# Kernel tuning notes

Hardware: AMD Instinct MI355X
Metric: run time of the kernel (lower is better)

## Reference

```python
import jax, jax.numpy as jnp
import numpy as np

NEG_INF = float('-inf')


def setup_inputs() -> dict:
    key = jax.random.key(0)
    ks = jax.random.split(key, 5)
    B, S, D = 2, 4096, 2048
    H, Hd, R = 16, 64, 64  # heads, head_dim, dq_rank
    ratio = 4
    sc = 0.02
    return {
        'hidden': jax.random.normal(ks[0], (B, S, D), jnp.float32),
        'w_dq': jax.random.normal(ks[1], (D, R), jnp.float32) * sc,
        'w_iuq': jax.random.normal(ks[2], (R, H * Hd), jnp.float32) * sc,
        'w_w': jax.random.normal(ks[3], (D, H), jnp.float32) * sc,
        'w_comp': jax.random.normal(ks[4], (ratio * D, Hd), jnp.float32) * sc,
        'compress_ratio': ratio,
        'index_topk': 256,
    }


def reference(hidden, w_dq, w_iuq, w_w, w_comp, compress_ratio, index_topk):
    B, S, D = hidden.shape
    r = int(compress_ratio)
    K = int(index_topk)
    P = S // r
    H = w_w.shape[1]
    Hd = w_iuq.shape[1] // H

    # mini-Compressor: linear over concatenated windows of r tokens -> [B,P,Hd]
    k_icomp = hidden.reshape(B, P, r * D) @ w_comp

    # low-rank query projection: [B,S,R] -> [B,S,H,Hd]
    q_i = ((hidden @ w_dq) @ w_iuq).reshape(B, S, H, Hd)
    w_i = hidden @ w_w  # [B,S,H]

    relu = jax.nn.relu(jnp.einsum('bshd,bpd->bshp', q_i, k_icomp))
    scores = jnp.einsum('bshp,bsh->bsp', relu, w_i)  # weighted head-sum

    # causal mask over compressed pool: pool s covers [s*r,(s+1)*r); allowed iff window end <= t
    t_idx = jnp.arange(S)[:, None]
    s_end = (jnp.arange(P)[None, :] + 1) * r - 1
    mask = jnp.where(s_end <= t_idx, 0.0, NEG_INF).astype(scores.dtype)
    scores = scores + mask[None]

    k_eff = min(K, P)
    topk_scores, topk_idxs = jax.lax.top_k(scores, k_eff)
    topk_idxs = jnp.where(jnp.isneginf(topk_scores), -1, topk_idxs)
    if k_eff < K:
        pad_i = jnp.full((B, S, K - k_eff), -1, topk_idxs.dtype)
        pad_s = jnp.full((B, S, K - k_eff), NEG_INF, topk_scores.dtype)
        topk_idxs = jnp.concatenate([topk_idxs, pad_i], axis=-1)
        topk_scores = jnp.concatenate([topk_scores, pad_s], axis=-1)
    return topk_idxs, topk_scores
```

## Files before the change

### kernel.cpp

```cpp
#include <hip/hip_runtime.h>

constexpr int S_    = 4096;
constexpr int D_    = 2048;
constexpr int H_    = 16;
constexpr int HD_   = 64;
constexpr int P_    = 1024;
constexpr int TOPK_ = 256;
constexpr int ROWS_ = 8192;

#define NEGINF (-__builtin_inff())
#define MASK_SENTINEL (-3.0e38f)

typedef __attribute__((ext_vector_type(8))) short bf16x8;
typedef __attribute__((ext_vector_type(4))) float f32x4;
typedef unsigned long long u64;

static __device__ __forceinline__ unsigned short f32_to_bf16_rne(float x) {
  unsigned u = __float_as_uint(x);
  u += 0x7FFFu + ((u >> 16) & 1u);
  return (unsigned short)(u >> 16);
}
static __device__ __forceinline__ float bf16_to_f32(unsigned short h) {
  return __uint_as_float(((unsigned)h) << 16);
}

static __device__ __forceinline__ void split8(const float4 a, const float4 b,
                                              bf16x8& hi, bf16x8& lo) {
  const float x[8] = {a.x, a.y, a.z, a.w, b.x, b.y, b.z, b.w};
#pragma unroll
  for (int i = 0; i < 8; ++i) {
    const unsigned u = __float_as_uint(x[i]);
    const float r = x[i] - __uint_as_float(u & 0xFFFF0000u);
    hi[i] = (short)(u >> 16);
    lo[i] = (short)(__float_as_uint(r) >> 16);
  }
}

__global__ void conv_w(const float* __restrict__ wdq, const float* __restrict__ ww,
                       const float* __restrict__ wc,
                       unsigned short* __restrict__ bdh, unsigned short* __restrict__ bdl,
                       unsigned short* __restrict__ bwh, unsigned short* __restrict__ bwl,
                       unsigned short* __restrict__ bch, unsigned short* __restrict__ bcl) {
  const int i = blockIdx.x * 256 + threadIdx.x;
  float x;
  unsigned short *oh, *ol;
  int oi;
  if (i < 131072) {
    const int n = i >> 11, k = i & 2047;
    x = wdq[(size_t)k * 64 + n]; oh = bdh; ol = bdl; oi = i;
  } else if (i < 163840) {
    const int j = i - 131072;
    const int n = j >> 11, k = j & 2047;
    x = ww[(size_t)k * 16 + n]; oh = bwh; ol = bwl; oi = j;
  } else {
    const int j = i - 163840;
    if (j >= 524288) return;
    const int n = j >> 13, k = j & 8191;
    x = wc[(size_t)k * 64 + n]; oh = bch; ol = bcl; oi = j;
  }
  const unsigned u = __float_as_uint(x);
  const float r = x - __uint_as_float(u & 0xFFFF0000u);
  oh[oi] = (unsigned short)(u >> 16);
  ol[oi] = (unsigned short)(__float_as_uint(r) >> 16);
}

__global__ __launch_bounds__(256) void mfma_a(
    const float* __restrict__ hid,
    const unsigned short* __restrict__ bdh, const unsigned short* __restrict__ bdl,
    const unsigned short* __restrict__ bwh, const unsigned short* __restrict__ bwl,
    float* __restrict__ part1,
    float* __restrict__ part3) {
  const int t = threadIdx.x;
  const int w = t >> 6, lane = t & 63;
  const int m = lane & 15, quad = lane >> 4;
  const int m0 = blockIdx.x << 6;
  const int z  = blockIdx.y;
  const int r0 = m0 + (w << 4);
  const int kb = z << 8;

  f32x4 acc[5];
#pragma unroll
  for (int i = 0; i < 5; ++i) acc[i] = f32x4{0.f, 0.f, 0.f, 0.f};

  const float* ap = hid + (size_t)(r0 + m) * D_ + kb + (quad << 3);

#pragma unroll 1
  for (int ks = 0; ks < 8; ++ks) {
    const int koff = ks << 5;
    const float4 a0 = *(const float4*)(ap + koff);
    const float4 a1 = *(const float4*)(ap + koff + 4);
    bf16x8 Ah, Al;
    split8(a0, a1, Ah, Al);
    const size_t kcol = (size_t)(kb + koff + (quad << 3));
#pragma unroll
    for (int nt = 0; nt < 4; ++nt) {
      const size_t bo = (size_t)((nt << 4) + m) * D_ + kcol;
      const bf16x8 Bh = *(const bf16x8*)(bdh + bo);
      const bf16x8 Bl = *(const bf16x8*)(bdl + bo);
      f32x4 c = acc[nt];
      c = __builtin_amdgcn_mfma_f32_16x16x32_bf16(Ah, Bh, c, 0, 0, 0);
      c = __builtin_amdgcn_mfma_f32_16x16x32_bf16(Al, Bh, c, 0, 0, 0);
      c = __builtin_amdgcn_mfma_f32_16x16x32_bf16(Ah, Bl, c, 0, 0, 0);
      acc[nt] = c;
    }
    {
      const size_t bo = (size_t)m * D_ + kcol;
      const bf16x8 Bh = *(const bf16x8*)(bwh + bo);
      const bf16x8 Bl = *(const bf16x8*)(bwl + bo);
      f32x4 c = acc[4];
      c = __builtin_amdgcn_mfma_f32_16x16x32_bf16(Ah, Bh, c, 0, 0, 0);
      c = __builtin_amdgcn_mfma_f32_16x16x32_bf16(Al, Bh, c, 0, 0, 0);
      c = __builtin_amdgcn_mfma_f32_16x16x32_bf16(Ah, Bl, c, 0, 0, 0);
      acc[4] = c;
    }
  }

  float* p1 = part1 + (size_t)z * (ROWS_ * 64);
#pragma unroll
  for (int nt = 0; nt < 4; ++nt)
#pragma unroll
    for (int i = 0; i < 4; ++i)
      p1[(size_t)(r0 + (quad << 2) + i) * 64 + (nt << 4) + m] = acc[nt][i];
  float* p3 = part3 + (size_t)z * (ROWS_ * H_);
#pragma unroll
  for (int i = 0; i < 4; ++i)
    p3[(size_t)(r0 + (quad << 2) + i) * H_ + m] = acc[4][i];
}

__global__ __launch_bounds__(256) void mfma_g4(
    const float* __restrict__ hid,
    const unsigned short* __restrict__ bch, const unsigned short* __restrict__ bcl,
    float* __restrict__ part4) {
  const int t = threadIdx.x;
  const int w = t >> 6, lane = t & 63;
  const int m = lane & 15, quad = lane >> 4;
  const int m0 = blockIdx.x << 6;
  const int z  = blockIdx.y;
  const int r0 = m0 + (w << 4);
  const int kb = z << 9;

  f32x4 acc[4];
#pragma unroll
  for (int i = 0; i < 4; ++i) acc[i] = f32x4{0.f, 0.f, 0.f, 0.f};

  const float* ap = hid + (size_t)(r0 + m) * 8192 + kb + (quad << 3);

#pragma unroll 1
  for (int ks = 0; ks < 16; ++ks) {
    const int koff = ks << 5;
    const float4 a0 = *(const float4*)(ap + koff);
    const float4 a1 = *(const float4*)(ap + koff + 4);
    bf16x8 Ah, Al;
    split8(a0, a1, Ah, Al);
    const size_t kcol = (size_t)(kb + koff + (quad << 3));
#pragma unroll
    for (int nt = 0; nt < 4; ++nt) {
      const size_t bo = (size_t)((nt << 4) + m) * 8192 + kcol;
      const bf16x8 Bh = *(const bf16x8*)(bch + bo);
      const bf16x8 Bl = *(const bf16x8*)(bcl + bo);
      f32x4 c = acc[nt];
      c = __builtin_amdgcn_mfma_f32_16x16x32_bf16(Ah, Bh, c, 0, 0, 0);
      c = __builtin_amdgcn_mfma_f32_16x16x32_bf16(Al, Bh, c, 0, 0, 0);
      c = __builtin_amdgcn_mfma_f32_16x16x32_bf16(Ah, Bl, c, 0, 0, 0);
      acc[nt] = c;
    }
  }

  float* p4 = part4 + (size_t)z * (2048 * 64);
#pragma unroll
  for (int nt = 0; nt < 4; ++nt)
#pragma unroll
    for (int i = 0; i < 4; ++i)
      p4[(size_t)(r0 + (quad << 2) + i) * 64 + (nt << 4) + m] = acc[nt][i];
}

__global__ __launch_bounds__(256) void gemm64_bs(const float* __restrict__ A,
                                                 const float* __restrict__ B,
                                                 unsigned short* __restrict__ Ch,
                                                 unsigned short* __restrict__ Cl,
                                                 int M, int N, int K) {
  const int t  = threadIdx.x;
  const int tx = t & 15, ty = t >> 4;
  const int n0 = blockIdx.x << 6;
  const int m0 = blockIdx.y << 6;

  __shared__ float As[16][68];
  __shared__ float Bs[16][64];
  float acc[4][4] = {};

  const int am = t >> 2, ak = (t & 3) << 2;
  const int bk = t >> 4, bn = (t & 15) << 2;
  const float* Ap = A + (size_t)(m0 + am) * K + ak;
  const float* Bp = B + (size_t)bk * N + n0 + bn;

  for (int kk = 0; kk < K; kk += 16) {
    const float4 a4 = *(const float4*)(Ap + kk);
    const float4 b4 = *(const float4*)(Bp + (size_t)kk * N);
    __syncthreads();
    As[ak + 0][am] = a4.x; As[ak + 1][am] = a4.y;
    As[ak + 2][am] = a4.z; As[ak + 3][am] = a4.w;
    *(float4*)&Bs[bk][bn] = b4;
    __syncthreads();
#pragma unroll
    for (int k = 0; k < 16; ++k) {
      const float4 av = *(const float4*)&As[k][ty << 2];
      const float4 bv = *(const float4*)&Bs[k][tx << 2];
      acc[0][0] += av.x * bv.x; acc[0][1] += av.x * bv.y; acc[0][2] += av.x * bv.z; acc[0][3] += av.x * bv.w;
      acc[1][0] += av.y * bv.x; acc[1][1] += av.y * bv.y; acc[1][2] += av.y * bv.z; acc[1][3] += av.y * bv.w;
      acc[2][0] += av.z * bv.x; acc[2][1] += av.z * bv.y; acc[2][2] += av.z * bv.z; acc[2][3] += av.z * bv.w;
      acc[3][0] += av.w * bv.x; acc[3][1] += av.w * bv.y; acc[3][2] += av.w * bv.z; acc[3][3] += av.w * bv.w;
    }
  }
#pragma unroll
  for (int i = 0; i < 4; ++i) {
    const size_t off = (size_t)(m0 + (ty << 2) + i) * N + n0 + (tx << 2);
    ushort4 hv, lv;
    float v;
    v = acc[i][0]; hv.x = f32_to_bf16_rne(v); lv.x = f32_to_bf16_rne(v - bf16_to_f32(hv.x));
    v = acc[i][1]; hv.y = f32_to_bf16_rne(v); lv.y = f32_to_bf16_rne(v - bf16_to_f32(hv.y));
    v = acc[i][2]; hv.z = f32_to_bf16_rne(v); lv.z = f32_to_bf16_rne(v - bf16_to_f32(hv.z));
    v = acc[i][3]; hv.w = f32_to_bf16_rne(v); lv.w = f32_to_bf16_rne(v - bf16_to_f32(hv.w));
    *(ushort4*)&Ch[off] = hv;
    *(ushort4*)&Cl[off] = lv;
  }
}

__global__ void reduce_both(const float* __restrict__ part1, float* __restrict__ out1,
                            const float* __restrict__ part3, float* __restrict__ out3) {
  const int i = blockIdx.x * blockDim.x + threadIdx.x;
  if (i < 524288) {
    float s = 0.f;
#pragma unroll
    for (int z = 0; z < 8; ++z) s += part1[(size_t)z * 524288 + i];
    out1[i] = s;
  } else {
    const int j = i - 524288;
    float s = 0.f;
#pragma unroll
    for (int z = 0; z < 8; ++z) s += part3[(size_t)z * 131072 + j];
    out3[j] = s;
  }
}

__global__ void reduce_k_split(const float* __restrict__ part,
                               unsigned short* __restrict__ kh,
                               unsigned short* __restrict__ kl) {
  const int i = blockIdx.x * blockDim.x + threadIdx.x;
  if (i >= 2048 * HD_) return;
  const int n = 2048 * HD_;
  float s = 0.f;
#pragma unroll
  for (int z = 0; z < 16; ++z) s += part[(size_t)z * n + i];
  const unsigned short h = f32_to_bf16_rne(s);
  kh[i] = h;
  kl[i] = f32_to_bf16_rne(s - bf16_to_f32(h));
}

__global__ __launch_bounds__(256, 4) void score_mfma(
    const unsigned short* __restrict__ qh,
    const unsigned short* __restrict__ ql,
    const float* __restrict__ wi,
    const unsigned short* __restrict__ kh,
    const unsigned short* __restrict__ kl,
    float* __restrict__ scores_out) {
  __shared__ float wis[16][17];

  const int t    = threadIdx.x;
  const int w    = t >> 6;
  const int lane = t & 63;
  const int m    = lane & 15;
  const int quad = lane >> 4;

  const int bid = blockIdx.x;
  const int lid = (bid & 7) * 160 + (bid >> 3);
  const int b   = lid >= 640;
  const int i   = lid - (b ? 640 : 0);
  int g, qq;
  if (i < 64)       { g = i;                     qq = 0; }
  else if (i < 192) { g = (i + 64) >> 1;         qq = (i + 64) & 1; }
  else if (i < 384) { const int u = i + 192; g = u / 3; qq = u - g * 3; }
  else              { g = (i + 384) >> 2;        qq = (i + 384) & 3; }

  const int row0 = (b << 12) | (g << 4);
  const int p0   = (qq << 8) + (w << 6);

  if (t < 64)
    *(float4*)&wis[t >> 2][(t & 3) << 2] =
        *(const float4*)(wi + (size_t)(row0 + (t >> 2)) * H_ + ((t & 3) << 2));
  __syncthreads();

  const size_t kbase = ((size_t)(b << 10) + p0 + m) * 64 + (quad << 3);
  bf16x8 Bh[4][2], Bl[4][2];
#pragma unroll
  for (int nt = 0; nt < 4; ++nt) {
    const size_t ko = kbase + (size_t)(nt << 4) * 64;
    Bh[nt][0] = *(const bf16x8*)(kh + ko);
    Bh[nt][1] = *(const bf16x8*)(kh + ko + 32);
    Bl[nt][0] = *(const bf16x8*)(kl + ko);
    Bl[nt][1] = *(const bf16x8*)(kl + ko + 32);
  }

  float acc[4][4];
#pragma unroll
  for (int nt = 0; nt < 4; ++nt)
#pragma unroll
    for (int r = 0; r < 4; ++r) acc[nt][r] = 0.f;

  const size_t qbase = (size_t)(row0 + m) * 1024 + (quad << 3);

#pragma unroll 1
  for (int h = 0; h < 16; ++h) {
    const size_t qo = qbase + (size_t)h * 64;
    const bf16x8 Ah0 = *(const bf16x8*)(qh + qo);
    const bf16x8 Ah1 = *(const bf16x8*)(qh + qo + 32);
    const bf16x8 Al0 = *(const bf16x8*)(ql + qo);
    const bf16x8 Al1 = *(const bf16x8*)(ql + qo + 32);
    float wreg[4];
#pragma unroll
    for (int r = 0; r < 4; ++r) wreg[r] = wis[(quad << 2) + r][h];
#pragma unroll
    for (int nt = 0; nt < 4; ++nt) {
      f32x4 c = {0.f, 0.f, 0.f, 0.f};
      c = __builtin_amdgcn_mfma_f32_16x16x32_bf16(Ah0, Bh[nt][0], c, 0, 0, 0);
      c = __builtin_amdgcn_mfma_f32_16x16x32_bf16(Ah1, Bh[nt][1], c, 0, 0, 0);
      c = __builtin_amdgcn_mfma_f32_16x16x32_bf16(Al0, Bh[nt][0], c, 0, 0, 0);
      c = __builtin_amdgcn_mfma_f32_16x16x32_bf16(Al1, Bh[nt][1], c, 0, 0, 0);
      c = __builtin_amdgcn_mfma_f32_16x16x32_bf16(Ah0, Bl[nt][0], c, 0, 0, 0);
      c = __builtin_amdgcn_mfma_f32_16x16x32_bf16(Ah1, Bl[nt][1], c, 0, 0, 0);
#pragma unroll
      for (int r = 0; r < 4; ++r)
        acc[nt][r] += wreg[r] * fmaxf(c[r], 0.f);
    }
  }

  float* so = scores_out + (size_t)(row0 + (quad << 2)) * 1024 + p0 + m;
#pragma unroll
  for (int r = 0; r < 4; ++r)
#pragma unroll
    for (int nt = 0; nt < 4; ++nt)
      so[(size_t)r * 1024 + (nt << 4)] = acc[nt][r];
}

template <int K2, int J2, int LM>
static __device__ __forceinline__ void substage(u64* E, int lane) {
  if constexpr (J2 >= 16) {
    constexpr int XM = J2 >> 4;
    const bool lower = (lane & XM) == 0;
#pragma unroll
    for (int v = 0; v < 16; ++v) {
      const int e = ((lane & LM) << 4) | v;
      const u64 p = __shfl_xor(E[v], XM, 64);
      const bool up = (e & K2) == 0;
      const bool keepmin = (up == lower);
      const u64 mn = (E[v] < p) ? E[v] : p;
      const u64 mx = (E[v] < p) ? p : E[v];
      E[v] = keepmin ? mn : mx;
    }
  } else {
#pragma unroll
    for (int v = 0; v < 16; ++v) {
      if ((v & J2) == 0) {
        const int e = ((lane & LM) << 4) | v;
        const bool up = (e & K2) == 0;
        const u64 a = E[v], b = E[v | J2];
        const u64 mn = (a < b) ? a : b;
        const u64 mx = (a < b) ? b : a;
        E[v]      = up ? mn : mx;
        E[v | J2] = up ? mx : mn;
      }
    }
  }
}

template <int K2, int J2, int LM>
static __device__ __forceinline__ void substages(u64* E, int lane) {
  substage<K2, J2, LM>(E, lane);
  if constexpr (J2 > 1) substages<K2, (J2 >> 1), LM>(E, lane);
}

template <int K2, int J2, int LM>
static __device__ __forceinline__ void substage2(u64* E, u64* F, int lane) {
  if constexpr (J2 >= 16) {
    constexpr int XM = J2 >> 4;
    const bool lower = (lane & XM) == 0;
#pragma unroll
    for (int v = 0; v < 16; ++v) {
      const int e = ((lane & LM) << 4) | v;
      const bool up = (e & K2) == 0;
      const bool keepmin = (up == lower);
      const u64 pE = __shfl_xor(E[v], XM, 64);
      const u64 pF = __shfl_xor(F[v], XM, 64);
      const u64 mnE = (E[v] < pE) ? E[v] : pE;
      const u64 mxE = (E[v] < pE) ? pE : E[v];
      const u64 mnF = (F[v] < pF) ? F[v] : pF;
      const u64 mxF = (F[v] < pF) ? pF : F[v];
      E[v] = keepmin ? mnE : mxE;
      F[v] = keepmin ? mnF : mxF;
    }
  } else {
#pragma unroll
    for (int v = 0; v < 16; ++v) {
      if ((v & J2) == 0) {
        const int e = ((lane & LM) << 4) | v;
        const bool up = (e & K2) == 0;
        const u64 aE = E[v], bE = E[v | J2];
        const u64 mnE = (aE < bE) ? aE : bE;
        const u64 mxE = (aE < bE) ? bE : aE;
        E[v]      = up ? mnE : mxE;
        E[v | J2] = up ? mxE : mnE;
        const u64 aF = F[v], bF = F[v | J2];
        const u64 mnF = (aF < bF) ? aF : bF;
        const u64 mxF = (aF < bF) ? bF : aF;
        F[v]      = up ? mnF : mxF;
        F[v | J2] = up ? mxF : mnF;
      }
    }
  }
}

template <int K2, int J2, int LM>
static __device__ __forceinline__ void substages2(u64* E, u64* F, int lane) {
  substage2<K2, J2, LM>(E, F, lane);
  if constexpr (J2 > 1) substages2<K2, (J2 >> 1), LM>(E, F, lane);
}

static __device__ __forceinline__ void load_enc(const float* __restrict__ sr,
                                                int ebase, int plim, u64* E) {
#pragma unroll
  for (int v4 = 0; v4 < 4; ++v4) {
    const float4 f = *(const float4*)(sr + (v4 << 2));
    const float sv[4] = {f.x, f.y, f.z, f.w};
#pragma unroll
    for (int j = 0; j < 4; ++j) {
      const int v = (v4 << 2) + j;
      const int e = ebase + v;
      const float sc = (e < plim) ? sv[j] : NEGINF;
      const unsigned u  = __float_as_uint(sc);
      const unsigned mm = (u & 0x80000000u) ? ~u : (u | 0x80000000u);
      E[v] = ((u64)(mm ^ 0xFFFFFFFFu) << 32) | (unsigned)e;
    }
  }
}

static __device__ __forceinline__ void dec_write(const u64* E, float* __restrict__ oi,
                                                 float* __restrict__ os) {
#pragma unroll
  for (int v4 = 0; v4 < 4; ++v4) {
    float vi[4], vs[4];
#pragma unroll
    for (int j = 0; j < 4; ++j) {
      const u64 kk = E[(v4 << 2) + j];
      const unsigned idx = (unsigned)kk;
      const unsigned mm  = (unsigned)(kk >> 32) ^ 0xFFFFFFFFu;
      const unsigned u   = (mm & 0x80000000u) ? (mm ^ 0x80000000u) : ~mm;
      const float sc = __uint_as_float(u);
      const bool masked = (sc == NEGINF);
      vi[j] = masked ? -1.0f : (float)idx;
      vs[j] = masked ? MASK_SENTINEL : sc;
    }
    *(float4*)&oi[v4 << 2] = make_float4(vi[0], vi[1], vi[2], vi[3]);
    *(float4*)&os[v4 << 2] = make_float4(vs[0], vs[1], vs[2], vs[3]);
  }
}

__global__ __launch_bounds__(256) void topk_tiered(
    const float* __restrict__ scores,
    float* __restrict__ out_idx, float* __restrict__ out_sc) {
  const int t    = threadIdx.x;
  const int w    = t >> 6;
  const int lane = t & 63;
  const int bid  = blockIdx.x;

  if (bid < 512) {
    const int i2   = (bid << 2) + w;
    const int jA   = i2 << 1;
    const int jB   = jA + 1;
    const int bA   = jA >> 11, sA = 2048 + (jA & 2047);
    const int bB   = jB >> 11, sB = 2048 + (jB & 2047);
    const int rowA = (bA << 12) + sA;
    const int rowB = (bB << 12) + sB;
    const int plimA = (sA + 1) >> 2;
    const int plimB = (sB + 1) >> 2;
    u64 E[16], F[16];
    load_enc(scores + (size_t)rowA * 1024 + (lane << 4), lane << 4, plimA, E);
    load_enc(scores + (size_t)rowB * 1024 + (lane << 4), lane << 4, plimB, F);
    substages2<2, 1, 63>(E, F, lane);
    substages2<4, 2, 63>(E, F, lane);
    substages2<8, 4, 63>(E, F, lane);
    substages2<16, 8, 63>(E, F, lane);
    substages2<32, 16, 63>(E, F, lane);
    substages2<64, 32, 63>(E, F, lane);
    substages2<128, 64, 63>(E, F, lane);
    substages2<256, 128, 63>(E, F, lane);
    substages2<512, 256, 63>(E, F, lane);
    substages2<1024, 512, 63>(E, F, lane);
    if (lane < 16) {
      const size_t obA = (size_t)rowA * TOPK_ + (lane << 4);
      dec_write(E, out_idx + obA, out_sc + obA);
      const size_t obB = (size_t)rowB * TOPK_ + (lane << 4);
      dec_write(F, out_idx + obB, out_sc + obB);
    }
  } else if (bid < 768) {
    const int qb   = bid - 512;
    const int g    = lane >> 5;
    const int l32  = lane & 31;
    const int j    = (qb << 3) + (w << 1) + g;
    const int b    = j >> 10;
    const int s    = 1024 + (j & 1023);
    const int row  = (b << 12) + s;
    const int plim = (s + 1) >> 2;
    u64 E[16];
    load_enc(scores + (size_t)row * 1024 + (l32 << 4), l32 << 4, plim, E);
    substages<2, 1, 31>(E, lane);
    substages<4, 2, 31>(E, lane);
    substages<8, 4, 31>(E, lane);
    substages<16, 8, 31>(E, lane);
    substages<32, 16, 31>(E, lane);
    substages<64, 32, 31>(E, lane);
    substages<128, 64, 31>(E, lane);
    substages<256, 128, 31>(E, lane);
    substages<512, 256, 31>(E, lane);
    if (l32 < 16) {
      const size_t ob = (size_t)row * TOPK_ + (l32 << 4);
      dec_write(E, out_idx + ob, out_sc + ob);
    }
  } else {
    const int qb   = bid - 768;
    const int g    = lane >> 4;
    const int l16  = lane & 15;
    const int j    = (qb << 4) + (w << 2) + g;
    const int b    = j >> 10;
    const int s    = j & 1023;
    const int row  = (b << 12) + s;
    const int plim = (s + 1) >> 2;
    u64 E[16];
    load_enc(scores + (size_t)row * 1024 + (l16 << 4), l16 << 4, plim, E);
    substages<2, 1, 15>(E, lane);
    substages<4, 2, 15>(E, lane);
    substages<8, 4, 15>(E, lane);
    substages<16, 8, 15>(E, lane);
    substages<32, 16, 15>(E, lane);
    substages<64, 32, 15>(E, lane);
    substages<128, 64, 15>(E, lane);
    substages<256, 128, 15>(E, lane);
    const size_t ob = (size_t)row * TOPK_ + (l16 << 4);
    dec_write(E, out_idx + ob, out_sc + ob);
  }
}

extern "C" void kernel_launch(void* const* d_in, const int* in_sizes, int n_in,
                              void* d_out, int out_size, void* d_ws, size_t ws_size,
                              hipStream_t stream) {
  const float* hidden = (const float*)d_in[0];
  const float* w_dq   = (const float*)d_in[1];
  const float* w_iuq  = (const float*)d_in[2];
  const float* w_w    = (const float*)d_in[3];
  const float* w_comp = (const float*)d_in[4];

  float* ws = (float*)d_ws;
  float* tmp_dq = ws;
  float* w_i    = tmp_dq + 524288;
  unsigned short* qh = (unsigned short*)(w_i + 131072);
  unsigned short* ql = qh + 8388608;
  unsigned short* kh = ql + 8388608;
  unsigned short* kl = kh + 131072;
  float* scores = (float*)(kl + 131072);
  unsigned short* bdh = (unsigned short*)(scores + 8388608);
  unsigned short* bdl = bdh + 131072;
  unsigned short* bwh = bdl + 131072;
  unsigned short* bwl = bwh + 32768;
  unsigned short* bch = bwl + 32768;
  unsigned short* bcl = bch + 524288;
  float* part1 = scores;
  float* part3 = part1 + 8 * 524288;
  float* part4 = part3 + 8 * 131072;

  conv_w<<<dim3(2688), 256, 0, stream>>>(w_dq, w_w, w_comp,
                                         bdh, bdl, bwh, bwl, bch, bcl);
  mfma_a<<<dim3(128, 8), 256, 0, stream>>>(hidden, bdh, bdl, bwh, bwl, part1, part3);
  reduce_both<<<dim3((524288 + 131072) / 256), 256, 0, stream>>>(part1, tmp_dq,
                                                                 part3, w_i);
  mfma_g4<<<dim3(32, 16), 256, 0, stream>>>(hidden, bch, bcl, part4);
  reduce_k_split<<<dim3(131072 / 256), 256, 0, stream>>>(part4, kh, kl);
  gemm64_bs<<<dim3(16, 128, 1), 256, 0, stream>>>(tmp_dq, w_iuq, qh, ql, ROWS_, 1024, 64);
  score_mfma<<<dim3(1280), 256, 0, stream>>>(qh, ql, w_i, kh, kl, scores);
  float* out_idx = (float*)d_out;
  float* out_sc  = out_idx + (size_t)ROWS_ * TOPK_;
  topk_tiered<<<dim3(896), 256, 0, stream>>>(scores, out_idx, out_sc);
}
```

Baseline: 336.7 us.

## Double split-K, prefetch A loads, merge reductions, split MFMA accumulator chains

Doubles the split-K factor of both projection GEMMs (mfma_a and mfma_g4) to launch more blocks. Each of their k-loops now prefetches the next A tile into registers one step ahead. The three partial-sum reductions are merged into one launch, and the partial buffers move into the q and score workspace regions. In score_mfma, each dependent chain of six MFMAs becomes two independent chains of three that are summed at the end, which shortens the dependency latency. The cost is twice the partial-sum memory traffic and reduction work, plus buffer aliasing that depends on launch order.

```diff
diff --git a/kernel.cpp b/kernel.cpp
--- a/kernel.cpp
+++ b/kernel.cpp
@@ -76,7 +76,7 @@
   const int m0 = blockIdx.x << 6;
   const int z  = blockIdx.y;
   const int r0 = m0 + (w << 4);
-  const int kb = z << 8;
+  const int kb = z << 7;
 
   f32x4 acc[5];
 #pragma unroll
@@ -84,14 +84,20 @@
 
   const float* ap = hid + (size_t)(r0 + m) * D_ + kb + (quad << 3);
 
+  float4 a0 = *(const float4*)(ap);
+  float4 a1 = *(const float4*)(ap + 4);
+
 #pragma unroll 1
-  for (int ks = 0; ks < 8; ++ks) {
-    const int koff = ks << 5;
-    const float4 a0 = *(const float4*)(ap + koff);
-    const float4 a1 = *(const float4*)(ap + koff + 4);
+  for (int ks = 0; ks < 4; ++ks) {
+    float4 n0, n1;
+    if (ks < 3) {
+      const int nxt = (ks + 1) << 5;
+      n0 = *(const float4*)(ap + nxt);
+      n1 = *(const float4*)(ap + nxt + 4);
+    }
     bf16x8 Ah, Al;
     split8(a0, a1, Ah, Al);
-    const size_t kcol = (size_t)(kb + koff + (quad << 3));
+    const size_t kcol = (size_t)(kb + (ks << 5) + (quad << 3));
 #pragma unroll
     for (int nt = 0; nt < 4; ++nt) {
       const size_t bo = (size_t)((nt << 4) + m) * D_ + kcol;
@@ -113,6 +119,7 @@
       c = __builtin_amdgcn_mfma_f32_16x16x32_bf16(Ah, Bl, c, 0, 0, 0);
       acc[4] = c;
     }
+    a0 = n0; a1 = n1;
   }
 
   float* p1 = part1 + (size_t)z * (ROWS_ * 64);
@@ -137,7 +144,7 @@
   const int m0 = blockIdx.x << 6;
   const int z  = blockIdx.y;
   const int r0 = m0 + (w << 4);
-  const int kb = z << 9;
+  const int kb = z << 8;
 
   f32x4 acc[4];
 #pragma unroll
@@ -145,14 +152,20 @@
 
   const float* ap = hid + (size_t)(r0 + m) * 8192 + kb + (quad << 3);
 
+  float4 a0 = *(const float4*)(ap);
+  float4 a1 = *(const float4*)(ap + 4);
+
 #pragma unroll 1
-  for (int ks = 0; ks < 16; ++ks) {
-    const int koff = ks << 5;
-    const float4 a0 = *(const float4*)(ap + koff);
-    const float4 a1 = *(const float4*)(ap + koff + 4);
+  for (int ks = 0; ks < 8; ++ks) {
+    float4 n0, n1;
+    if (ks < 7) {
+      const int nxt = (ks + 1) << 5;
+      n0 = *(const float4*)(ap + nxt);
+      n1 = *(const float4*)(ap + nxt + 4);
+    }
     bf16x8 Ah, Al;
     split8(a0, a1, Ah, Al);
-    const size_t kcol = (size_t)(kb + koff + (quad << 3));
+    const size_t kcol = (size_t)(kb + (ks << 5) + (quad << 3));
 #pragma unroll
     for (int nt = 0; nt < 4; ++nt) {
       const size_t bo = (size_t)((nt << 4) + m) * 8192 + kcol;
@@ -164,6 +177,7 @@
       c = __builtin_amdgcn_mfma_f32_16x16x32_bf16(Ah, Bl, c, 0, 0, 0);
       acc[nt] = c;
     }
+    a0 = n0; a1 = n1;
   }
 
   float* p4 = part4 + (size_t)z * (2048 * 64);
@@ -225,35 +239,32 @@
   }
 }
 
-__global__ void reduce_both(const float* __restrict__ part1, float* __restrict__ out1,
-                            const float* __restrict__ part3, float* __restrict__ out3) {
+__global__ void reduce_all(const float* __restrict__ part1, float* __restrict__ out1,
+                           const float* __restrict__ part3, float* __restrict__ out3,
+                           const float* __restrict__ part4,
+                           unsigned short* __restrict__ kh,
+                           unsigned short* __restrict__ kl) {
   const int i = blockIdx.x * blockDim.x + threadIdx.x;
   if (i < 524288) {
     float s = 0.f;
 #pragma unroll
-    for (int z = 0; z < 8; ++z) s += part1[(size_t)z * 524288 + i];
+    for (int z = 0; z < 16; ++z) s += part1[(size_t)z * 524288 + i];
     out1[i] = s;
-  } else {
+  } else if (i < 655360) {
     const int j = i - 524288;
     float s = 0.f;
 #pragma unroll
-    for (int z = 0; z < 8; ++z) s += part3[(size_t)z * 131072 + j];
+    for (int z = 0; z < 16; ++z) s += part3[(size_t)z * 131072 + j];
     out3[j] = s;
-  }
-}
-
-__global__ void reduce_k_split(const float* __restrict__ part,
-                               unsigned short* __restrict__ kh,
-                               unsigned short* __restrict__ kl) {
-  const int i = blockIdx.x * blockDim.x + threadIdx.x;
-  if (i >= 2048 * HD_) return;
-  const int n = 2048 * HD_;
-  float s = 0.f;
-#pragma unroll
-  for (int z = 0; z < 16; ++z) s += part[(size_t)z * n + i];
-  const unsigned short h = f32_to_bf16_rne(s);
-  kh[i] = h;
-  kl[i] = f32_to_bf16_rne(s - bf16_to_f32(h));
+  } else {
+    const int j = i - 655360;
+    float s = 0.f;
+#pragma unroll
+    for (int z = 0; z < 32; ++z) s += part4[(size_t)z * 131072 + j];
+    const unsigned short h = f32_to_bf16_rne(s);
+    kh[j] = h;
+    kl[j] = f32_to_bf16_rne(s - bf16_to_f32(h));
+  }
 }
 
 __global__ __launch_bounds__(256, 4) void score_mfma(
@@ -320,16 +331,17 @@
     for (int r = 0; r < 4; ++r) wreg[r] = wis[(quad << 2) + r][h];
 #pragma unroll
     for (int nt = 0; nt < 4; ++nt) {
-      f32x4 c = {0.f, 0.f, 0.f, 0.f};
-      c = __builtin_amdgcn_mfma_f32_16x16x32_bf16(Ah0, Bh[nt][0], c, 0, 0, 0);
-      c = __builtin_amdgcn_mfma_f32_16x16x32_bf16(Ah1, Bh[nt][1], c, 0, 0, 0);
-      c = __builtin_amdgcn_mfma_f32_16x16x32_bf16(Al0, Bh[nt][0], c, 0, 0, 0);
-      c = __builtin_amdgcn_mfma_f32_16x16x32_bf16(Al1, Bh[nt][1], c, 0, 0, 0);
-      c = __builtin_amdgcn_mfma_f32_16x16x32_bf16(Ah0, Bl[nt][0], c, 0, 0, 0);
-      c = __builtin_amdgcn_mfma_f32_16x16x32_bf16(Ah1, Bl[nt][1], c, 0, 0, 0);
+      f32x4 c0 = {0.f, 0.f, 0.f, 0.f};
+      f32x4 c1 = {0.f, 0.f, 0.f, 0.f};
+      c0 = __builtin_amdgcn_mfma_f32_16x16x32_bf16(Ah0, Bh[nt][0], c0, 0, 0, 0);
+      c1 = __builtin_amdgcn_mfma_f32_16x16x32_bf16(Ah1, Bh[nt][1], c1, 0, 0, 0);
+      c0 = __builtin_amdgcn_mfma_f32_16x16x32_bf16(Al0, Bh[nt][0], c0, 0, 0, 0);
+      c1 = __builtin_amdgcn_mfma_f32_16x16x32_bf16(Al1, Bh[nt][1], c1, 0, 0, 0);
+      c0 = __builtin_amdgcn_mfma_f32_16x16x32_bf16(Ah0, Bl[nt][0], c0, 0, 0, 0);
+      c1 = __builtin_amdgcn_mfma_f32_16x16x32_bf16(Ah1, Bl[nt][1], c1, 0, 0, 0);
 #pragma unroll
       for (int r = 0; r < 4; ++r)
-        acc[nt][r] += wreg[r] * fmaxf(c[r], 0.f);
+        acc[nt][r] += wreg[r] * fmaxf(c0[r] + c1[r], 0.f);
     }
   }
 
@@ -572,16 +584,15 @@
   unsigned short* bch = bwl + 32768;
   unsigned short* bcl = bch + 524288;
   float* part1 = scores;
-  float* part3 = part1 + 8 * 524288;
-  float* part4 = part3 + 8 * 131072;
+  float* part4 = (float*)qh;
+  float* part3 = (float*)ql;
 
   conv_w<<<dim3(2688), 256, 0, stream>>>(w_dq, w_w, w_comp,
                                          bdh, bdl, bwh, bwl, bch, bcl);
-  mfma_a<<<dim3(128, 8), 256, 0, stream>>>(hidden, bdh, bdl, bwh, bwl, part1, part3);
-  reduce_both<<<dim3((524288 + 131072) / 256), 256, 0, stream>>>(part1, tmp_dq,
-                                                                 part3, w_i);
-  mfma_g4<<<dim3(32, 16), 256, 0, stream>>>(hidden, bch, bcl, part4);
-  reduce_k_split<<<dim3(131072 / 256), 256, 0, stream>>>(part4, kh, kl);
+  mfma_a<<<dim3(128, 16), 256, 0, stream>>>(hidden, bdh, bdl, bwh, bwl, part1, part3);
+  mfma_g4<<<dim3(32, 32), 256, 0, stream>>>(hidden, bch, bcl, part4);
+  reduce_all<<<dim3(3072), 256, 0, stream>>>(part1, tmp_dq, part3, w_i,
+                                             part4, kh, kl);
   gemm64_bs<<<dim3(16, 128, 1), 256, 0, stream>>>(tmp_dq, w_iuq, qh, ql, ROWS_, 1024, 64);
   score_mfma<<<dim3(1280), 256, 0, stream>>>(qh, ql, w_i, kh, kl, scores);
   float* out_idx = (float*)d_out;
```

Result: slower. 353.7 us (+5.1%).
